# Performance work log

Hardware: AMD Instinct MI355X
Metric: run time of the kernel (lower is better)

The kernel has to match this reference:

```python
import jax, jax.numpy as jnp
import numpy as np

B, S, D_IN, D_H = 4, 2048, 1024, 1024

def setup_inputs() -> dict:
    key = jax.random.key(0)
    k1, k2, k3, k4 = jax.random.split(key, 4)
    x = jax.random.normal(k1, (B, S, D_IN), dtype=jnp.float32)
    # torch nn.Linear weights are [out, in]; kept in that layout
    Wq = jax.random.normal(k2, (D_H, D_IN), dtype=jnp.float32) * (1.0 / np.sqrt(D_IN))
    Wk = jax.random.normal(k3, (D_H, D_IN), dtype=jnp.float32) * (1.0 / np.sqrt(D_IN))
    Wv = jax.random.normal(k4, (D_H, D_IN), dtype=jnp.float32) * (1.0 / np.sqrt(D_IN))
    return {"x": x, "Wq": Wq, "Wk": Wk, "Wv": Wv}

def reference(x, Wq, Wk, Wv):
    # projections (Linear, no bias): x @ W.T
    q = jnp.einsum('bsd,hd->bsh', x, Wq)
    k = jnp.einsum('bsd,hd->bsh', x, Wk)
    v = jnp.einsum('bsd,hd->bsh', x, Wv)
    scores = jnp.einsum('bqh,bkh->bqk', q, k)  # [B,S,S]
    S_len = x.shape[1]
    causal = jnp.triu(jnp.ones((S_len, S_len), dtype=bool), k=1)
    scores = jnp.where(causal, -jnp.inf, scores) / jnp.sqrt(jnp.float32(k.shape[-1]))
    attn = jax.nn.softmax(scores, axis=-1)
    # dropout is identity in eval/deterministic mode
    return jnp.einsum('bqk,bkh->bqh', attn, v)
```

## Files before the change

### kernel.cpp

```cpp
#include <hip/hip_runtime.h>
#include <hip/hip_bf16.h>
#include <stdint.h>

typedef unsigned short u16;
typedef __attribute__((ext_vector_type(8))) short short8;
typedef __attribute__((ext_vector_type(4))) float f32x4;
typedef __attribute__((ext_vector_type(4))) u16 u16x4;

#define S_LEN 2048
#define D_DIM 1024
#define NBATCH 4
#define BM 128
#define BN 128
#define BK 32

enum { MODE_QKV = 0, MODE_SC = 2, MODE_PV = 3 };

__device__ inline u16 f2bf(float f) {
  uint32_t u = __float_as_uint(f);
  uint32_t r = (u + 0x7fffu + ((u >> 16) & 1u)) >> 16;
  return (u16)r;
}

__global__ __launch_bounds__(256) void cast_all(
    const float* __restrict__ x, const float* __restrict__ wq,
    const float* __restrict__ wk, const float* __restrict__ wv,
    u16* __restrict__ out) {
  const int X4 = (NBATCH * S_LEN * D_DIM) / 4;
  const int W4 = (D_DIM * D_DIM) / 4;
  const int total = X4 + 3 * W4;
  int g = blockIdx.x * blockDim.x + threadIdx.x;
  int stride = gridDim.x * blockDim.x;
  for (; g < total; g += stride) {
    const float* src;
    int si;
    if (g < X4) { src = x; si = g; }
    else if (g < X4 + W4) { src = wq; si = g - X4; }
    else if (g < X4 + 2 * W4) { src = wk; si = g - X4 - W4; }
    else { src = wv; si = g - X4 - 2 * W4; }
    f32x4 v = *reinterpret_cast<const f32x4*>(src + (long)si * 4);
    u16x4 o;
    o[0] = f2bf(v[0]); o[1] = f2bf(v[1]); o[2] = f2bf(v[2]); o[3] = f2bf(v[3]);
    *reinterpret_cast<u16x4*>(out + (long)g * 4) = o;
  }
}

template <int MODE>
__global__ __launch_bounds__(256, 2) void gemm_bt(
    const u16* __restrict__ A, const u16* __restrict__ B, void* __restrict__ C,
    int K, long strideAb, long strideBb, long strideCb, int ldc,
    float* __restrict__ aux, int nb) {
  __shared__ u16 As[2][BM * BK];
  __shared__ u16 Bs[2][BN * BK];
  __shared__ float ilds[BM];

  int br, bc, bz;
  if (MODE == MODE_SC) {
    int t;
    if (nb == NBATCH) {
      int lin = blockIdx.x;
      int xcd = lin & 7;
      bz = xcd >> 1;
      t = (xcd & 1) * 68 + (lin >> 3);
    } else {
      bz = blockIdx.z;
      t = blockIdx.x;
    }
    int r = (int)((sqrtf(8.0f * (float)t + 1.0f) - 1.0f) * 0.5f);
    while ((r + 1) * (r + 2) / 2 <= t) ++r;
    while (r * (r + 1) / 2 > t) --r;
    br = r;
    bc = t - r * (r + 1) / 2;
  } else if (MODE == MODE_PV) {
    int xr, bcl, ch;
    if (nb == NBATCH) {
      int lin = blockIdx.x;
      int xcd = lin & 7;
      bz = xcd >> 1;
      ch = xcd & 1;
      int rank = lin >> 3;
      xr = rank >> 2;
      bcl = rank & 3;
    } else {
      bz = blockIdx.z;
      xr = blockIdx.x;
      ch = 0;
      bcl = blockIdx.y;
    }
    int nt = S_LEN / BM;
    br = (xr & 1) ? (xr >> 1) : (nt - 1 - (xr >> 1));
    bc = (nb == NBATCH) ? (ch * 4 + bcl) : bcl;
  } else {
    int lin = blockIdx.y * gridDim.x + blockIdx.x;
    int xcd = lin & 7;
    int rank = lin >> 3;
    br = xcd * 8 + (rank & 7);
    bc = rank >> 3;
    bz = 0;
  }

  const u16* Ab = A + (long)bz * strideAb;
  const u16* Bb = B + (long)bz * strideBb;

  const int rowBase = br * BM;
  const int colBase = bc * BN;
  int nkt = (MODE == MODE_PV) ? (br + 1) * (BM / BK) : (K / BK);

  const int tid = threadIdx.x;
  const int lane = tid & 63;
  const int wave = tid >> 6;
  const int wr = wave >> 1, wc = wave & 1;

  if (MODE == MODE_PV) {
    int row = tid >> 1, half = tid & 1;
    const float* lp = aux + (long)bz * S_LEN * 32 + (long)(rowBase + row) * 32;
    int nslot = 2 * (br + 1);
    float s = 0.f;
    for (int k = half; k < nslot; k += 2) s += lp[k];
    s += __shfl_xor(s, 1);
    if (half == 0) ilds[row] = 1.f / s;
  }

  f32x4 acc[4][4];
#pragma unroll
  for (int i = 0; i < 4; i++)
#pragma unroll
    for (int j = 0; j < 4; j++) acc[i][j] = f32x4{0.f, 0.f, 0.f, 0.f};

  const int srow = tid >> 2;
  const int skc = (tid & 3) * 8;

  auto stage = [&](int buf, int kt) {
    const u16* ga = Ab + (long)(rowBase + srow) * K + kt * BK + skc;
    const u16* gb = Bb + (long)(colBase + srow) * K + kt * BK + skc;
    __builtin_amdgcn_global_load_lds(
        (const __attribute__((address_space(1))) void*)ga,
        (__attribute__((address_space(3))) void*)(&As[buf][tid * 8]), 16, 0, 0);
    __builtin_amdgcn_global_load_lds(
        (const __attribute__((address_space(1))) void*)(ga + (long)64 * K),
        (__attribute__((address_space(3))) void*)(&As[buf][64 * BK + tid * 8]), 16, 0, 0);
    __builtin_amdgcn_global_load_lds(
        (const __attribute__((address_space(1))) void*)gb,
        (__attribute__((address_space(3))) void*)(&Bs[buf][tid * 8]), 16, 0, 0);
    __builtin_amdgcn_global_load_lds(
        (const __attribute__((address_space(1))) void*)(gb + (long)64 * K),
        (__attribute__((address_space(3))) void*)(&Bs[buf][64 * BK + tid * 8]), 16, 0, 0);
  };

  stage(0, 0);
  __syncthreads();
  int cur = 0;
  for (int kt = 0; kt < nkt; ++kt) {
    if (kt + 1 < nkt) stage(cur ^ 1, kt + 1);
    short8 af[4], bf[4];
#pragma unroll
    for (int i = 0; i < 4; i++)
      af[i] = *reinterpret_cast<const short8*>(
          &As[cur][(wr * 64 + i * 16 + (lane & 15)) * BK + (lane >> 4) * 8]);
#pragma unroll
    for (int j = 0; j < 4; j++)
      bf[j] = *reinterpret_cast<const short8*>(
          &Bs[cur][(wc * 64 + j * 16 + (lane & 15)) * BK + (lane >> 4) * 8]);
#pragma unroll
    for (int i = 0; i < 4; i++)
#pragma unroll
      for (int j = 0; j < 4; j++)
        acc[i][j] = __builtin_amdgcn_mfma_f32_16x16x32_bf16(af[i], bf[j], acc[i][j], 0, 0, 0);
    __syncthreads();
    cur ^= 1;
  }

  const int lr = (lane >> 4) * 4;
  const int lc = lane & 15;

  if (MODE == MODE_QKV) {
    u16* Cb = (u16*)C;
    const long seg = (long)NBATCH * S_LEN * D_DIM;
    const int segi = colBase >> 10;
    const int hb = colBase & 1023;
    if (segi < 2) {
      u16* dst = Cb + (long)segi * seg;
#pragma unroll
      for (int i = 0; i < 4; i++) {
        int r0 = rowBase + wr * 64 + i * 16 + lr;
#pragma unroll
        for (int j = 0; j < 4; j++) {
          int c0 = hb + wc * 64 + j * 16 + lc;
#pragma unroll
          for (int q = 0; q < 4; q++) dst[(long)(r0 + q) * D_DIM + c0] = f2bf(acc[i][j][q]);
        }
      }
    } else {
      u16* dst = Cb + 2 * seg;
#pragma unroll
      for (int i = 0; i < 4; i++) {
        int m0 = rowBase + wr * 64 + i * 16 + lr;
        int b = m0 >> 11, s0 = m0 & (S_LEN - 1);
#pragma unroll
        for (int j = 0; j < 4; j++) {
          int h = hb + wc * 64 + j * 16 + lc;
          u16x4 o;
          o[0] = f2bf(acc[i][j][0]); o[1] = f2bf(acc[i][j][1]);
          o[2] = f2bf(acc[i][j][2]); o[3] = f2bf(acc[i][j][3]);
          *reinterpret_cast<u16x4*>(dst + ((long)b * D_DIM + h) * S_LEN + s0) = o;
        }
      }
    }
  } else if (MODE == MODE_SC) {
    u16* Cb = (u16*)C + (long)bz * strideCb;
    float* lp = aux + (long)bz * S_LEN * 32;
#pragma unroll
    for (int i = 0; i < 4; i++) {
      int r0 = rowBase + wr * 64 + i * 16 + lr;
#pragma unroll
      for (int q = 0; q < 4; q++) {
        int r = r0 + q;
        float rs = 0.f;
#pragma unroll
        for (int j = 0; j < 4; j++) {
          int c0 = colBase + wc * 64 + j * 16 + lc;
          float p = (c0 <= r) ? __expf(acc[i][j][q] * 0.03125f - 8.f) : 0.f;
          rs += p;
          Cb[(long)r * ldc + c0] = f2bf(p);
        }
#pragma unroll
        for (int off = 1; off < 16; off <<= 1) rs += __shfl_xor(rs, off);
        if ((lane & 15) == 0) lp[r * 32 + bc * 2 + wc] = rs;
      }
    }
  } else {
    float* Cb = (float*)C + (long)bz * strideCb;
#pragma unroll
    for (int i = 0; i < 4; i++) {
      int r0 = rowBase + wr * 64 + i * 16 + lr;
#pragma unroll
      for (int j = 0; j < 4; j++) {
        int c0 = colBase + wc * 64 + j * 16 + lc;
#pragma unroll
        for (int q = 0; q < 4; q++)
          Cb[(long)(r0 + q) * ldc + c0] = acc[i][j][q] * ilds[wr * 64 + i * 16 + lr + q];
      }
    }
  }
}

extern "C" void kernel_launch(void* const* d_in, const int* in_sizes, int n_in,
                              void* d_out, int out_size, void* d_ws, size_t ws_size,
                              hipStream_t stream) {
  const float* x = (const float*)d_in[0];
  const float* Wq = (const float*)d_in[1];
  const float* Wk = (const float*)d_in[2];
  const float* Wv = (const float*)d_in[3];
  float* out = (float*)d_out;

  const size_t SD = (size_t)S_LEN * D_DIM;
  const size_t SS = (size_t)S_LEN * S_LEN;
  const size_t DD = (size_t)D_DIM * D_DIM;

  size_t off = 0;
  char* ws = (char*)d_ws;
  auto alloc = [&](size_t bytes) -> char* {
    char* p = ws + off;
    off += (bytes + 255) & ~(size_t)255;
    return p;
  };
  u16* xb = (u16*)alloc((NBATCH * SD + 3 * DD) * 2);
  u16* Wqkvb = xb + NBATCH * SD;
  u16* QKVt = (u16*)alloc(3 * NBATCH * SD * 2);
  u16* Qb = QKVt;
  u16* Kb = QKVt + NBATCH * SD;
  u16* Vt = QKVt + 2 * NBATCH * SD;
  size_t base_off = off;
  size_t need_full = base_off + ((NBATCH * SS * 2 + 255) & ~(size_t)255) +
                     ((NBATCH * (size_t)S_LEN * 32 * 4 + 255) & ~(size_t)255);
  const int nbpar = (ws_size >= need_full) ? NBATCH : 1;
  u16* P = (u16*)alloc((size_t)nbpar * SS * 2);
  float* l_part = (float*)alloc((size_t)nbpar * S_LEN * 32 * 4);

  cast_all<<<2048, 256, 0, stream>>>(x, Wq, Wk, Wv, xb);

  dim3 gp((NBATCH * S_LEN) / BM, 3 * D_DIM / BN, 1);
  gemm_bt<MODE_QKV><<<gp, 256, 0, stream>>>(xb, Wqkvb, QKVt, D_DIM, 0, 0, 0, D_DIM,
                                            nullptr, NBATCH);

  const int ntri = (S_LEN / BM) * (S_LEN / BM + 1) / 2;
  if (nbpar == NBATCH) {
    gemm_bt<MODE_SC><<<dim3(8 * 68, 1, 1), 256, 0, stream>>>(
        Qb, Kb, P, D_DIM, (long)SD, (long)SD, (long)SS, S_LEN, l_part, NBATCH);
    gemm_bt<MODE_PV><<<dim3(8 * 64, 1, 1), 256, 0, stream>>>(
        P, Vt, out, S_LEN, (long)SS, (long)SD, (long)SD, D_DIM, l_part, NBATCH);
  } else {
    for (int b = 0; b < NBATCH; ++b) {
      gemm_bt<MODE_SC><<<dim3(ntri, 1, 1), 256, 0, stream>>>(
          Qb + b * SD, Kb + b * SD, P, D_DIM, 0, 0, 0, S_LEN, l_part, 1);
      gemm_bt<MODE_PV><<<dim3(S_LEN / BM, D_DIM / BN, 1), 256, 0, stream>>>(
          P, Vt + b * SD, out + b * SD, S_LEN, 0, 0, 0, D_DIM, l_part, 1);
    }
  }
}
```

Measured before the change: 155.0 us.

## Load B operand fragments directly from global into registers, bypassing LDS

```diff
diff --git a/kernel.cpp b/kernel.cpp
--- a/kernel.cpp
+++ b/kernel.cpp
@@ -51,7 +51,6 @@
     int K, long strideAb, long strideBb, long strideCb, int ldc,
     float* __restrict__ aux, int nb) {
   __shared__ u16 As[2][BM * BK];
-  __shared__ u16 Bs[2][BN * BK];
   __shared__ float ilds[BM];
 
   int br, bc, bz;
@@ -110,6 +109,8 @@
   const int lane = tid & 63;
   const int wave = tid >> 6;
   const int wr = wave >> 1, wc = wave & 1;
+  const int l15 = lane & 15;
+  const int g = lane >> 4;
 
   if (MODE == MODE_PV) {
     int row = tid >> 1, half = tid & 1;
@@ -132,46 +133,57 @@
 
   auto stage = [&](int buf, int kt) {
     const u16* ga = Ab + (long)(rowBase + srow) * K + kt * BK + skc;
-    const u16* gb = Bb + (long)(colBase + srow) * K + kt * BK + skc;
     __builtin_amdgcn_global_load_lds(
         (const __attribute__((address_space(1))) void*)ga,
         (__attribute__((address_space(3))) void*)(&As[buf][tid * 8]), 16, 0, 0);
     __builtin_amdgcn_global_load_lds(
         (const __attribute__((address_space(1))) void*)(ga + (long)64 * K),
         (__attribute__((address_space(3))) void*)(&As[buf][64 * BK + tid * 8]), 16, 0, 0);
-    __builtin_amdgcn_global_load_lds(
-        (const __attribute__((address_space(1))) void*)gb,
-        (__attribute__((address_space(3))) void*)(&Bs[buf][tid * 8]), 16, 0, 0);
-    __builtin_amdgcn_global_load_lds(
-        (const __attribute__((address_space(1))) void*)(gb + (long)64 * K),
-        (__attribute__((address_space(3))) void*)(&Bs[buf][64 * BK + tid * 8]), 16, 0, 0);
-  };
-
+  };
+
+  const u16* Bfb = Bb + (long)(colBase + wc * 64 + l15) * K + g * 8;
+  auto loadB = [&](short8* d, int kt) {
+#pragma unroll
+    for (int j = 0; j < 4; j++)
+      d[j] = *reinterpret_cast<const short8*>(Bfb + (long)(j * 16) * K + kt * BK);
+  };
+
+  auto rdA = [&](short8* d, int buf) {
+#pragma unroll
+    for (int i = 0; i < 4; i++)
+      d[i] = *reinterpret_cast<const short8*>(
+          &As[buf][(wr * 64 + i * 16 + l15) * BK + g * 8]);
+  };
+  auto mm = [&](const short8* af, const short8* bf) {
+#pragma unroll
+    for (int i = 0; i < 4; i++)
+#pragma unroll
+      for (int j = 0; j < 4; j++)
+        acc[i][j] = __builtin_amdgcn_mfma_f32_16x16x32_bf16(af[i], bf[j], acc[i][j], 0, 0, 0);
+  };
+
+  short8 bf0[4], bf1[4], af[4];
+  loadB(bf0, 0);
   stage(0, 0);
   __syncthreads();
   int cur = 0;
-  for (int kt = 0; kt < nkt; ++kt) {
-    if (kt + 1 < nkt) stage(cur ^ 1, kt + 1);
-    short8 af[4], bf[4];
-#pragma unroll
-    for (int i = 0; i < 4; i++)
-      af[i] = *reinterpret_cast<const short8*>(
-          &As[cur][(wr * 64 + i * 16 + (lane & 15)) * BK + (lane >> 4) * 8]);
-#pragma unroll
-    for (int j = 0; j < 4; j++)
-      bf[j] = *reinterpret_cast<const short8*>(
-          &Bs[cur][(wc * 64 + j * 16 + (lane & 15)) * BK + (lane >> 4) * 8]);
-#pragma unroll
-    for (int i = 0; i < 4; i++)
-#pragma unroll
-      for (int j = 0; j < 4; j++)
-        acc[i][j] = __builtin_amdgcn_mfma_f32_16x16x32_bf16(af[i], bf[j], acc[i][j], 0, 0, 0);
+  for (int kt = 0; kt < nkt; kt += 2) {
+    if (kt + 1 < nkt) { stage(cur ^ 1, kt + 1); loadB(bf1, kt + 1); }
+    rdA(af, cur);
+    mm(af, bf0);
     __syncthreads();
     cur ^= 1;
-  }
-
-  const int lr = (lane >> 4) * 4;
-  const int lc = lane & 15;
+    if (kt + 1 < nkt) {
+      if (kt + 2 < nkt) { stage(cur ^ 1, kt + 2); loadB(bf0, kt + 2); }
+      rdA(af, cur);
+      mm(af, bf1);
+      __syncthreads();
+      cur ^= 1;
+    }
+  }
+
+  const int lr = g * 4;
+  const int lc = l15;
 
   if (MODE == MODE_QKV) {
     u16* Cb = (u16*)C;
```

New measurement: 248.5 us. +60.3%, slower.
